# Kernel optimization log

Measured on AMD Instinct MI355X. Metric: run time of the kernel, lower is better.

## Reference

```python
import jax, jax.numpy as jnp
import numpy as np


def _species_mlp(x, W1, b1, W2, b2, W3, b3, W4, b4):
    # x: [S, A, F] per-species feature blocks; weights: [S, ...] per-species MLPs
    h = jax.nn.silu(jnp.einsum('saf,sfh->sah', x, W1) + b1[:, None, :])
    h = jax.nn.silu(jnp.einsum('sah,shk->sak', h, W2) + b2[:, None, :])
    h = jax.nn.silu(jnp.einsum('sak,skm->sam', h, W3) + b3[:, None, :])
    e = jnp.einsum('sam,smo->sao', h, W4) + b4[:, None, :]  # [S, A, 1]
    return e[..., 0]  # atomic energies [S, A]


def setup_inputs() -> dict:
    key = jax.random.key(0)
    ks = jax.random.split(key, 12)
    S, A, F, H = 4, 32768, 512, 256
    n_structures = 512
    w = 0.05  # keep activations in a sane range
    return {
        'features': jax.random.normal(ks[0], (S, A, F), dtype=jnp.float32),
        'struct_ids': jax.random.randint(ks[1], (S, A), 0, n_structures),
        'W1': jax.random.normal(ks[2], (S, F, H), dtype=jnp.float32) * w,
        'b1': jax.random.normal(ks[3], (S, H), dtype=jnp.float32) * w,
        'W2': jax.random.normal(ks[4], (S, H, H), dtype=jnp.float32) * w,
        'b2': jax.random.normal(ks[5], (S, H), dtype=jnp.float32) * w,
        'W3': jax.random.normal(ks[6], (S, H, H), dtype=jnp.float32) * w,
        'b3': jax.random.normal(ks[7], (S, H), dtype=jnp.float32) * w,
        'W4': jax.random.normal(ks[8], (S, H, 1), dtype=jnp.float32) * w,
        'b4': jax.random.normal(ks[9], (S, 1), dtype=jnp.float32) * w,
        'energy_shift': jax.random.normal(ks[10], (1,), dtype=jnp.float32),
        'n_structures': n_structures,
    }


def reference(features, struct_ids, W1, b1, W2, b2, W3, b3, W4, b4, energy_shift, n_structures):
    # per-species MLP over all blocks (the per-species gather is the block layout itself)
    atomic_energies = _species_mlp(features, W1, b1, W2, b2, W3, b3, W4, b4)  # [S, A]
    # index_add scatter of atomic energies into per-structure energies
    energies = jax.ops.segment_sum(
        atomic_energies.reshape(-1), struct_ids.reshape(-1), num_segments=n_structures
    )
    energies = energies + energy_shift[0]
    return energies
```

## Files before the change

kernel.cpp:

```cpp
#include <hip/hip_runtime.h>

typedef _Float16 f16x8 __attribute__((ext_vector_type(8)));
typedef _Float16 f16x4 __attribute__((ext_vector_type(4)));
typedef float f32x4 __attribute__((ext_vector_type(4)));

static constexpr int S = 4;
static constexpr int NATOMS = 32768;
static constexpr int FIN = 512;
static constexpr int H = 256;
static constexpr int BM = 128;
static constexpr int XSTR = 36;
static constexpr int HSTR = 264;
static constexpr int NSTRUCT = 512;
static constexpr int RBLK = 128;
static constexpr int APB = (S * NATOMS) / RBLK;

__global__ void pack_w(const float* __restrict__ W, _Float16* __restrict__ dst, int KT) {
    int idx = blockIdx.x * 256 + threadIdx.x;
    int j = idx & 7;
    int lane = (idx >> 3) & 63;
    int rest = idx >> 9;
    int kt = rest % KT;
    int t2 = rest / KT;
    int K = KT * 32;
    int k = kt * 32 + (lane >> 4) * 8 + j;
    int ntile = t2 & 15;
    int s = t2 >> 4;
    int n = ntile * 16 + (lane & 15);
    int p = kt * 4 + (ntile & 3);
    size_t o = ((((size_t)(s * 4 + (ntile >> 2))) * (KT * 4) + p) * 64 + lane) * 8 + j;
    dst[o] = (_Float16)W[((size_t)s * K + k) * H + n];
}

__global__ __launch_bounds__(512, 3) void fused_mlp(
    const float* __restrict__ X,
    const _Float16* __restrict__ W1p, const _Float16* __restrict__ W2p,
    const _Float16* __restrict__ W3p,
    const float* __restrict__ b1, const float* __restrict__ b2,
    const float* __restrict__ b3,
    const float* __restrict__ W4, const float* __restrict__ b4,
    float* __restrict__ Eout)
{
    __shared__ _Float16 smem[BM * HSTR];
    __shared__ float e_lds[4][BM];

    const int s = blockIdx.y;
    const int tile = blockIdx.x;
    const int tid = threadIdx.x;
    const int rw = __builtin_amdgcn_readfirstlane(tid >> 6);
    const int wm = rw >> 2;
    const int wn = rw & 3;
    const int lane = tid & 63;
    const int g = lane >> 4;
    const int mh = lane & 15;
    const int srow = tid >> 2;
    const int cq = tid & 3;

    const float* Xb = X + (size_t)(s * NATOMS + tile * BM) * FIN;
    _Float16* hb = smem;

    const _Float16* Wb1 = W1p + ((size_t)(s * 4 + wn)) * (64 * 512) + lane * 8;
    const _Float16* Wb2 = W2p + ((size_t)(s * 4 + wn)) * (32 * 512) + lane * 8;
    const _Float16* Wb3 = W3p + ((size_t)(s * 4 + wn)) * (32 * 512) + lane * 8;

    f32x4 acc[4][4];
#pragma unroll
    for (int i = 0; i < 4; ++i)
#pragma unroll
        for (int j = 0; j < 4; ++j)
            acc[i][j] = f32x4{0.f, 0.f, 0.f, 0.f};

    f32x4 ld[3][2];
    auto loadc = [&](int slot, int c) {
        const float* p = Xb + (size_t)srow * FIN + c * 32 + cq * 8;
        ld[slot][0] = *(const f32x4*)(p);
        ld[slot][1] = *(const f32x4*)(p + 4);
    };
    auto storec = [&](int slot, int c) {
        _Float16* xb = smem + (c % 3) * (BM * XSTR);
#pragma unroll
        for (int i = 0; i < 2; ++i) {
            f16x4 v;
#pragma unroll
            for (int j = 0; j < 4; ++j) v[j] = (_Float16)ld[slot][i][j];
            *(f16x4*)(xb + srow * XSTR + cq * 8 + i * 4) = v;
        }
    };
    auto l1mfma = [&](int c) {
        const _Float16* xb = smem + (c % 3) * (BM * XSTR);
        f16x8 a[4];
#pragma unroll
        for (int mt = 0; mt < 4; ++mt)
            a[mt] = *(const f16x8*)(xb + (wm * 64 + mt * 16 + mh) * XSTR + g * 8);
        __builtin_amdgcn_s_setprio(1);
#pragma unroll
        for (int nt = 0; nt < 4; ++nt) {
            f16x8 b = *(const f16x8*)(Wb1 + (c * 4 + nt) * 512);
#pragma unroll
            for (int mt = 0; mt < 4; ++mt)
                acc[mt][nt] = __builtin_amdgcn_mfma_f32_16x16x32_f16(a[mt], b, acc[mt][nt], 0, 0, 0);
        }
        __builtin_amdgcn_s_setprio(0);
    };

    loadc(0, 0);
    loadc(1, 1);
    loadc(2, 2);
    storec(0, 0);
    asm volatile("s_waitcnt lgkmcnt(0)" ::: "memory");
    __builtin_amdgcn_s_barrier();
#pragma unroll
    for (int c = 0; c < 16; ++c) {
        if (c < 15) storec((c + 1) % 3, c + 1);
        if (c < 13) loadc(c % 3, c + 3);
        l1mfma(c);
        asm volatile("s_waitcnt lgkmcnt(0)" ::: "memory");
        __builtin_amdgcn_s_barrier();
    }
    __syncthreads();

    {
        float bv[4];
#pragma unroll
        for (int nt = 0; nt < 4; ++nt) bv[nt] = b1[s * H + wn * 64 + nt * 16 + mh];
#pragma unroll
        for (int mt = 0; mt < 4; ++mt)
#pragma unroll
            for (int nt = 0; nt < 4; ++nt)
#pragma unroll
                for (int r = 0; r < 4; ++r) {
                    float v = acc[mt][nt][r] + bv[nt];
                    v = __fdividef(v, 1.f + __expf(-v));
                    hb[(wm * 64 + mt * 16 + g * 4 + r) * HSTR + wn * 64 + nt * 16 + mh] = (_Float16)v;
                    acc[mt][nt][r] = 0.f;
                }
    }
    __syncthreads();

    for (int l = 0; l < 2; ++l) {
        const _Float16* Wb = l ? Wb3 : Wb2;
#pragma unroll
        for (int ks = 0; ks < 8; ++ks) {
            f16x8 a[4];
#pragma unroll
            for (int mt = 0; mt < 4; ++mt)
                a[mt] = *(const f16x8*)(hb + (wm * 64 + mt * 16 + mh) * HSTR + ks * 32 + g * 8);
            __builtin_amdgcn_s_setprio(1);
#pragma unroll
            for (int nt = 0; nt < 4; ++nt) {
                f16x8 b = *(const f16x8*)(Wb + (ks * 4 + nt) * 512);
#pragma unroll
                for (int mt = 0; mt < 4; ++mt)
                    acc[mt][nt] = __builtin_amdgcn_mfma_f32_16x16x32_f16(a[mt], b, acc[mt][nt], 0, 0, 0);
            }
            __builtin_amdgcn_s_setprio(0);
        }
        __syncthreads();
        if (l == 0) {
            float bv[4];
#pragma unroll
            for (int nt = 0; nt < 4; ++nt) bv[nt] = b2[s * H + wn * 64 + nt * 16 + mh];
#pragma unroll
            for (int mt = 0; mt < 4; ++mt)
#pragma unroll
                for (int nt = 0; nt < 4; ++nt)
#pragma unroll
                    for (int r = 0; r < 4; ++r) {
                        float v = acc[mt][nt][r] + bv[nt];
                        v = __fdividef(v, 1.f + __expf(-v));
                        hb[(wm * 64 + mt * 16 + g * 4 + r) * HSTR + wn * 64 + nt * 16 + mh] = (_Float16)v;
                        acc[mt][nt][r] = 0.f;
                    }
            __syncthreads();
        }
    }

    {
        float bv[4], w4v[4];
#pragma unroll
        for (int nt = 0; nt < 4; ++nt) {
            int col = wn * 64 + nt * 16 + mh;
            bv[nt] = b3[s * H + col];
            w4v[nt] = W4[s * H + col];
        }
#pragma unroll
        for (int mt = 0; mt < 4; ++mt)
#pragma unroll
            for (int r = 0; r < 4; ++r) {
                float v = 0.f;
#pragma unroll
                for (int nt = 0; nt < 4; ++nt) {
                    float h = acc[mt][nt][r] + bv[nt];
                    h = __fdividef(h, 1.f + __expf(-h));
                    v += h * w4v[nt];
                }
                v += __shfl_xor(v, 1);
                v += __shfl_xor(v, 2);
                v += __shfl_xor(v, 4);
                v += __shfl_xor(v, 8);
                if (mh == r) e_lds[wn][wm * 64 + mt * 16 + g * 4 + r] = v;
            }
    }
    __syncthreads();
    if (tid < BM) {
        float e = b4[s] + e_lds[0][tid] + e_lds[1][tid] + e_lds[2][tid] + e_lds[3][tid];
        Eout[(size_t)s * NATOMS + tile * BM + tid] = e;
    }
}

__global__ __launch_bounds__(256) void reduce1(
    const float* __restrict__ E, const int* __restrict__ ids,
    float* __restrict__ partials)
{
    __shared__ float tbl[NSTRUCT];
    const int b = blockIdx.x;
    const int tid = threadIdx.x;
    tbl[tid] = 0.f;
    tbl[tid + 256] = 0.f;
    __syncthreads();
    const int base = b * APB;
#pragma unroll
    for (int i = 0; i < APB / 256; ++i) {
        int a = base + i * 256 + tid;
        atomicAdd(&tbl[ids[a]], E[a]);
    }
    __syncthreads();
    partials[(size_t)b * NSTRUCT + tid] = tbl[tid];
    partials[(size_t)b * NSTRUCT + tid + 256] = tbl[tid + 256];
}

__global__ __launch_bounds__(512) void reduce2(
    const float* __restrict__ partials, const float* __restrict__ shift,
    float* __restrict__ out)
{
    const int i = threadIdx.x;
    float v = shift[0];
#pragma unroll 8
    for (int b = 0; b < RBLK; ++b) v += partials[(size_t)b * NSTRUCT + i];
    out[i] = v;
}

extern "C" void kernel_launch(void* const* d_in, const int* in_sizes, int n_in,
                              void* d_out, int out_size, void* d_ws, size_t ws_size,
                              hipStream_t stream) {
    const float* X   = (const float*)d_in[0];
    const int*   ids = (const int*)d_in[1];
    const float* W1  = (const float*)d_in[2];
    const float* b1  = (const float*)d_in[3];
    const float* W2  = (const float*)d_in[4];
    const float* b2  = (const float*)d_in[5];
    const float* W3  = (const float*)d_in[6];
    const float* b3  = (const float*)d_in[7];
    const float* W4  = (const float*)d_in[8];
    const float* b4  = (const float*)d_in[9];
    const float* shift = (const float*)d_in[10];

    _Float16* W1p = (_Float16*)d_ws;
    _Float16* W2p = W1p + (size_t)S * 4 * 64 * 512;
    _Float16* W3p = W2p + (size_t)S * 4 * 32 * 512;
    float* E = (float*)(W3p + (size_t)S * 4 * 32 * 512);
    float* partials = E + (size_t)S * NATOMS;

    pack_w<<<2048, 256, 0, stream>>>(W1, W1p, 16);
    pack_w<<<1024, 256, 0, stream>>>(W2, W2p, 8);
    pack_w<<<1024, 256, 0, stream>>>(W3, W3p, 8);

    dim3 grid(NATOMS / BM, S);
    fused_mlp<<<grid, 512, 0, stream>>>(X, W1p, W2p, W3p, b1, b2, b3, W4, b4, E);

    reduce1<<<RBLK, 256, 0, stream>>>(E, ids, partials);
    reduce2<<<1, 512, 0, stream>>>(partials, shift, (float*)d_out);
}
```

Measured before the change: 155.9 us.

## Split fused MLP into separate layer-1 GEMM and layers 2-4 kernels

Splits the single fused per-tile MLP kernel into two launches. The first streams X and computes layer 1 with SiLU, writing fp16 activations to a global workspace. The second reloads those activations into LDS and runs layers 2 through 4. Each kernel now needs less LDS than the fused one, which may allow more concurrent blocks or better scheduling. The cost is an extra global write and read of a 128K x 256 fp16 activation buffer plus one more kernel launch.

```diff
diff --git a/kernel.cpp b/kernel.cpp
--- a/kernel.cpp
+++ b/kernel.cpp
@@ -32,17 +32,11 @@
     dst[o] = (_Float16)W[((size_t)s * K + k) * H + n];
 }
 
-__global__ __launch_bounds__(512, 3) void fused_mlp(
-    const float* __restrict__ X,
-    const _Float16* __restrict__ W1p, const _Float16* __restrict__ W2p,
-    const _Float16* __restrict__ W3p,
-    const float* __restrict__ b1, const float* __restrict__ b2,
-    const float* __restrict__ b3,
-    const float* __restrict__ W4, const float* __restrict__ b4,
-    float* __restrict__ Eout)
+__global__ __launch_bounds__(512, 3) void l1gemm(
+    const float* __restrict__ X, const _Float16* __restrict__ W1p,
+    const float* __restrict__ b1, _Float16* __restrict__ h1)
 {
-    __shared__ _Float16 smem[BM * HSTR];
-    __shared__ float e_lds[4][BM];
+    __shared__ _Float16 xlds[3 * BM * XSTR];
 
     const int s = blockIdx.y;
     const int tile = blockIdx.x;
@@ -57,11 +51,7 @@
     const int cq = tid & 3;
 
     const float* Xb = X + (size_t)(s * NATOMS + tile * BM) * FIN;
-    _Float16* hb = smem;
-
     const _Float16* Wb1 = W1p + ((size_t)(s * 4 + wn)) * (64 * 512) + lane * 8;
-    const _Float16* Wb2 = W2p + ((size_t)(s * 4 + wn)) * (32 * 512) + lane * 8;
-    const _Float16* Wb3 = W3p + ((size_t)(s * 4 + wn)) * (32 * 512) + lane * 8;
 
     f32x4 acc[4][4];
 #pragma unroll
@@ -77,7 +67,7 @@
         ld[slot][1] = *(const f32x4*)(p + 4);
     };
     auto storec = [&](int slot, int c) {
-        _Float16* xb = smem + (c % 3) * (BM * XSTR);
+        _Float16* xb = xlds + (c % 3) * (BM * XSTR);
 #pragma unroll
         for (int i = 0; i < 2; ++i) {
             f16x4 v;
@@ -87,7 +77,7 @@
         }
     };
     auto l1mfma = [&](int c) {
-        const _Float16* xb = smem + (c % 3) * (BM * XSTR);
+        const _Float16* xb = xlds + (c % 3) * (BM * XSTR);
         f16x8 a[4];
 #pragma unroll
         for (int mt = 0; mt < 4; ++mt)
@@ -117,25 +107,62 @@
         asm volatile("s_waitcnt lgkmcnt(0)" ::: "memory");
         __builtin_amdgcn_s_barrier();
     }
+
+    _Float16* Ho = h1 + ((size_t)(s * NATOMS + tile * BM)) * H;
+    float bv[4];
+#pragma unroll
+    for (int nt = 0; nt < 4; ++nt) bv[nt] = b1[s * H + wn * 64 + nt * 16 + mh];
+#pragma unroll
+    for (int mt = 0; mt < 4; ++mt)
+#pragma unroll
+        for (int nt = 0; nt < 4; ++nt)
+#pragma unroll
+            for (int r = 0; r < 4; ++r) {
+                float v = acc[mt][nt][r] + bv[nt];
+                v = __fdividef(v, 1.f + __expf(-v));
+                Ho[(size_t)(wm * 64 + mt * 16 + g * 4 + r) * H + wn * 64 + nt * 16 + mh] = (_Float16)v;
+            }
+}
+
+__global__ __launch_bounds__(512, 3) void l234(
+    const _Float16* __restrict__ h1,
+    const _Float16* __restrict__ W2p, const _Float16* __restrict__ W3p,
+    const float* __restrict__ b2, const float* __restrict__ b3,
+    const float* __restrict__ W4, const float* __restrict__ b4,
+    float* __restrict__ Eout)
+{
+    __shared__ _Float16 hb[BM * HSTR];
+    __shared__ float e_lds[4][BM];
+
+    const int s = blockIdx.y;
+    const int tile = blockIdx.x;
+    const int tid = threadIdx.x;
+    const int rw = __builtin_amdgcn_readfirstlane(tid >> 6);
+    const int wm = rw >> 2;
+    const int wn = rw & 3;
+    const int lane = tid & 63;
+    const int g = lane >> 4;
+    const int mh = lane & 15;
+
+    const _Float16* Wb2 = W2p + ((size_t)(s * 4 + wn)) * (32 * 512) + lane * 8;
+    const _Float16* Wb3 = W3p + ((size_t)(s * 4 + wn)) * (32 * 512) + lane * 8;
+
+    const _Float16* Hb = h1 + ((size_t)(s * NATOMS + tile * BM)) * H;
+#pragma unroll
+    for (int i = 0; i < 8; ++i) {
+        int gi = i * 512 + tid;
+        int row = gi >> 5, gr = gi & 31;
+        f16x8 v = *(const f16x8*)(Hb + (size_t)row * H + gr * 8);
+        *(f16x8*)(hb + row * HSTR + gr * 8) = v;
+    }
     __syncthreads();
 
-    {
-        float bv[4];
-#pragma unroll
-        for (int nt = 0; nt < 4; ++nt) bv[nt] = b1[s * H + wn * 64 + nt * 16 + mh];
-#pragma unroll
-        for (int mt = 0; mt < 4; ++mt)
-#pragma unroll
-            for (int nt = 0; nt < 4; ++nt)
-#pragma unroll
-                for (int r = 0; r < 4; ++r) {
-                    float v = acc[mt][nt][r] + bv[nt];
-                    v = __fdividef(v, 1.f + __expf(-v));
-                    hb[(wm * 64 + mt * 16 + g * 4 + r) * HSTR + wn * 64 + nt * 16 + mh] = (_Float16)v;
-                    acc[mt][nt][r] = 0.f;
-                }
-    }
-    __syncthreads();
+    f32x4 acc[4][4];
+#pragma unroll
+    for (int i = 0; i < 4; ++i)
+#pragma unroll
+        for (int j = 0; j < 4; ++j)
+            acc[i][j] = f32x4{0.f, 0.f, 0.f, 0.f};
 
     for (int l = 0; l < 2; ++l) {
         const _Float16* Wb = l ? Wb3 : Wb2;
@@ -260,13 +287,15 @@
     _Float16* W3p = W2p + (size_t)S * 4 * 32 * 512;
     float* E = (float*)(W3p + (size_t)S * 4 * 32 * 512);
     float* partials = E + (size_t)S * NATOMS;
+    _Float16* h1 = (_Float16*)(partials + (size_t)RBLK * NSTRUCT);
 
     pack_w<<<2048, 256, 0, stream>>>(W1, W1p, 16);
     pack_w<<<1024, 256, 0, stream>>>(W2, W2p, 8);
     pack_w<<<1024, 256, 0, stream>>>(W3, W3p, 8);
 
     dim3 grid(NATOMS / BM, S);
-    fused_mlp<<<grid, 512, 0, stream>>>(X, W1p, W2p, W3p, b1, b2, b3, W4, b4, E);
+    l1gemm<<<grid, 512, 0, stream>>>(X, W1p, b1, h1);
+    l234<<<grid, 512, 0, stream>>>(h1, W2p, W3p, b2, b3, W4, b4, E);
 
     reduce1<<<RBLK, 256, 0, stream>>>(E, ids, partials);
     reduce2<<<1, 512, 0, stream>>>(partials, shift, (float*)d_out);
```

Measured after the change: 177.6 us. +13.9%, slower.

## Switch MLP matmuls to 32x32x16 MFMA with swizzled hidden-layer LDS layout

Applied to the files above, without the earlier changes.

Replaces the 16x16x32 f16 MFMA tiling with 32x32x16 MFMA tiles (2x2 per wave), repacking weights to match the new operand layout. The hidden activation buffer in shared memory is now XOR-swizzled by row group to avoid bank conflicts on the new access pattern. The goal is fewer A/B operand loads per FLOP and higher MFMA throughput. The trade-off is larger per-lane accumulator vectors, which may raise register pressure under the 3-block launch bound, and a longer final reduction over 32 lanes.

```diff
diff --git a/kernel.cpp b/kernel.cpp
--- a/kernel.cpp
+++ b/kernel.cpp
@@ -3,6 +3,7 @@
 typedef _Float16 f16x8 __attribute__((ext_vector_type(8)));
 typedef _Float16 f16x4 __attribute__((ext_vector_type(4)));
 typedef float f32x4 __attribute__((ext_vector_type(4)));
+typedef float f32x16 __attribute__((ext_vector_type(16)));
 
 static constexpr int S = 4;
 static constexpr int NATOMS = 32768;
@@ -15,21 +16,19 @@
 static constexpr int RBLK = 128;
 static constexpr int APB = (S * NATOMS) / RBLK;
 
-__global__ void pack_w(const float* __restrict__ W, _Float16* __restrict__ dst, int KT) {
+__global__ void pack_w32(const float* __restrict__ W, _Float16* __restrict__ dst, int P) {
     int idx = blockIdx.x * 256 + threadIdx.x;
     int j = idx & 7;
     int lane = (idx >> 3) & 63;
-    int rest = idx >> 9;
-    int kt = rest % KT;
-    int t2 = rest / KT;
-    int K = KT * 32;
-    int k = kt * 32 + (lane >> 4) * 8 + j;
-    int ntile = t2 & 15;
-    int s = t2 >> 4;
-    int n = ntile * 16 + (lane & 15);
-    int p = kt * 4 + (ntile & 3);
-    size_t o = ((((size_t)(s * 4 + (ntile >> 2))) * (KT * 4) + p) * 64 + lane) * 8 + j;
-    dst[o] = (_Float16)W[((size_t)s * K + k) * H + n];
+    int p = (idx >> 9) % P;
+    int t = (idx >> 9) / P;
+    int wn = t & 3;
+    int s = t >> 2;
+    int K = P * 8;
+    int c = p >> 2, kk = (p >> 1) & 1, nt = p & 1;
+    int k = (c * 2 + kk) * 16 + (lane >> 5) * 8 + j;
+    int n = wn * 64 + nt * 32 + (lane & 31);
+    dst[((size_t)idx & ~511) + lane * 8 + j] = (_Float16)W[((size_t)s * K + k) * H + n];
 }
 
 __global__ __launch_bounds__(512, 3) void fused_mlp(
@@ -51,8 +50,8 @@
     const int wm = rw >> 2;
     const int wn = rw & 3;
     const int lane = tid & 63;
-    const int g = lane >> 4;
-    const int mh = lane & 15;
+    const int c32 = lane & 31;
+    const int hi = lane >> 5;
     const int srow = tid >> 2;
     const int cq = tid & 3;
 
@@ -63,12 +62,12 @@
     const _Float16* Wb2 = W2p + ((size_t)(s * 4 + wn)) * (32 * 512) + lane * 8;
     const _Float16* Wb3 = W3p + ((size_t)(s * 4 + wn)) * (32 * 512) + lane * 8;
 
-    f32x4 acc[4][4];
-#pragma unroll
-    for (int i = 0; i < 4; ++i)
-#pragma unroll
-        for (int j = 0; j < 4; ++j)
-            acc[i][j] = f32x4{0.f, 0.f, 0.f, 0.f};
+    f32x16 acc[2][2];
+#pragma unroll
+    for (int i = 0; i < 2; ++i)
+#pragma unroll
+        for (int j = 0; j < 2; ++j)
+            acc[i][j] = (f32x16)(0.f);
 
     f32x4 ld[3][2];
     auto loadc = [&](int slot, int c) {
@@ -88,19 +87,22 @@
     };
     auto l1mfma = [&](int c) {
         const _Float16* xb = smem + (c % 3) * (BM * XSTR);
-        f16x8 a[4];
-#pragma unroll
-        for (int mt = 0; mt < 4; ++mt)
-            a[mt] = *(const f16x8*)(xb + (wm * 64 + mt * 16 + mh) * XSTR + g * 8);
-        __builtin_amdgcn_s_setprio(1);
-#pragma unroll
-        for (int nt = 0; nt < 4; ++nt) {
-            f16x8 b = *(const f16x8*)(Wb1 + (c * 4 + nt) * 512);
-#pragma unroll
-            for (int mt = 0; mt < 4; ++mt)
-                acc[mt][nt] = __builtin_amdgcn_mfma_f32_16x16x32_f16(a[mt], b, acc[mt][nt], 0, 0, 0);
-        }
-        __builtin_amdgcn_s_setprio(0);
+#pragma unroll
+        for (int kk = 0; kk < 2; ++kk) {
+            f16x8 a[2];
+#pragma unroll
+            for (int mt = 0; mt < 2; ++mt)
+                a[mt] = *(const f16x8*)(xb + (wm * 64 + mt * 32 + c32) * XSTR + kk * 16 + hi * 8);
+            __builtin_amdgcn_s_setprio(1);
+#pragma unroll
+            for (int nt = 0; nt < 2; ++nt) {
+                f16x8 b = *(const f16x8*)(Wb1 + ((c * 4 + kk * 2 + nt)) * 512);
+#pragma unroll
+                for (int mt = 0; mt < 2; ++mt)
+                    acc[mt][nt] = __builtin_amdgcn_mfma_f32_32x32x16_f16(a[mt], b, acc[mt][nt], 0, 0, 0);
+            }
+            __builtin_amdgcn_s_setprio(0);
+        }
     };
 
     loadc(0, 0);
@@ -119,86 +121,83 @@
     }
     __syncthreads();
 
-    {
-        float bv[4];
-#pragma unroll
-        for (int nt = 0; nt < 4; ++nt) bv[nt] = b1[s * H + wn * 64 + nt * 16 + mh];
-#pragma unroll
-        for (int mt = 0; mt < 4; ++mt)
-#pragma unroll
-            for (int nt = 0; nt < 4; ++nt)
-#pragma unroll
-                for (int r = 0; r < 4; ++r) {
-                    float v = acc[mt][nt][r] + bv[nt];
+    auto hwrite = [&](int grow, int col, float v) {
+        int g8 = (col >> 3) ^ ((grow >> 3) & 3);
+        hb[grow * HSTR + (g8 << 3) + (col & 7)] = (_Float16)v;
+    };
+    auto silu_epi = [&](const float* bias) {
+#pragma unroll
+        for (int nt = 0; nt < 2; ++nt) {
+            float bv = bias[s * H + wn * 64 + nt * 32 + c32];
+#pragma unroll
+            for (int mt = 0; mt < 2; ++mt)
+#pragma unroll
+                for (int r = 0; r < 16; ++r) {
+                    float v = acc[mt][nt][r] + bv;
                     v = __fdividef(v, 1.f + __expf(-v));
-                    hb[(wm * 64 + mt * 16 + g * 4 + r) * HSTR + wn * 64 + nt * 16 + mh] = (_Float16)v;
+                    int grow = wm * 64 + mt * 32 + (r & 3) + 8 * (r >> 2) + 4 * hi;
+                    hwrite(grow, wn * 64 + nt * 32 + c32, v);
                     acc[mt][nt][r] = 0.f;
                 }
-    }
+        }
+    };
+
+    silu_epi(b1);
     __syncthreads();
 
     for (int l = 0; l < 2; ++l) {
         const _Float16* Wb = l ? Wb3 : Wb2;
 #pragma unroll
         for (int ks = 0; ks < 8; ++ks) {
-            f16x8 a[4];
-#pragma unroll
-            for (int mt = 0; mt < 4; ++mt)
-                a[mt] = *(const f16x8*)(hb + (wm * 64 + mt * 16 + mh) * HSTR + ks * 32 + g * 8);
-            __builtin_amdgcn_s_setprio(1);
-#pragma unroll
-            for (int nt = 0; nt < 4; ++nt) {
-                f16x8 b = *(const f16x8*)(Wb + (ks * 4 + nt) * 512);
-#pragma unroll
-                for (int mt = 0; mt < 4; ++mt)
-                    acc[mt][nt] = __builtin_amdgcn_mfma_f32_16x16x32_f16(a[mt], b, acc[mt][nt], 0, 0, 0);
+#pragma unroll
+            for (int kk = 0; kk < 2; ++kk) {
+                f16x8 a[2];
+#pragma unroll
+                for (int mt = 0; mt < 2; ++mt) {
+                    int grow = wm * 64 + mt * 32 + c32;
+                    int g8 = (ks * 4 + kk * 2 + hi) ^ ((grow >> 3) & 3);
+                    a[mt] = *(const f16x8*)(hb + grow * HSTR + (g8 << 3));
+                }
+                __builtin_amdgcn_s_setprio(1);
+#pragma unroll
+                for (int nt = 0; nt < 2; ++nt) {
+                    f16x8 b = *(const f16x8*)(Wb + ((ks * 4 + kk * 2 + nt)) * 512);
+#pragma unroll
+                    for (int mt = 0; mt < 2; ++mt)
+                        acc[mt][nt] = __builtin_amdgcn_mfma_f32_32x32x16_f16(a[mt], b, acc[mt][nt], 0, 0, 0);
+                }
+                __builtin_amdgcn_s_setprio(0);
             }
-            __builtin_amdgcn_s_setprio(0);
         }
         __syncthreads();
         if (l == 0) {
-            float bv[4];
-#pragma unroll
-            for (int nt = 0; nt < 4; ++nt) bv[nt] = b2[s * H + wn * 64 + nt * 16 + mh];
-#pragma unroll
-            for (int mt = 0; mt < 4; ++mt)
-#pragma unroll
-                for (int nt = 0; nt < 4; ++nt)
-#pragma unroll
-                    for (int r = 0; r < 4; ++r) {
-                        float v = acc[mt][nt][r] + bv[nt];
-                        v = __fdividef(v, 1.f + __expf(-v));
-                        hb[(wm * 64 + mt * 16 + g * 4 + r) * HSTR + wn * 64 + nt * 16 + mh] = (_Float16)v;
-                        acc[mt][nt][r] = 0.f;
-                    }
+            silu_epi(b2);
             __syncthreads();
         }
     }
 
     {
-        float bv[4], w4v[4];
-#pragma unroll
-        for (int nt = 0; nt < 4; ++nt) {
-            int col = wn * 64 + nt * 16 + mh;
-            bv[nt] = b3[s * H + col];
-            w4v[nt] = W4[s * H + col];
-        }
-#pragma unroll
-        for (int mt = 0; mt < 4; ++mt)
-#pragma unroll
-            for (int r = 0; r < 4; ++r) {
+#pragma unroll
+        for (int mt = 0; mt < 2; ++mt)
+#pragma unroll
+            for (int r = 0; r < 16; ++r) {
                 float v = 0.f;
 #pragma unroll
-                for (int nt = 0; nt < 4; ++nt) {
-                    float h = acc[mt][nt][r] + bv[nt];
+                for (int nt = 0; nt < 2; ++nt) {
+                    int col = wn * 64 + nt * 32 + c32;
+                    float h = acc[mt][nt][r] + b3[s * H + col];
                     h = __fdividef(h, 1.f + __expf(-h));
-                    v += h * w4v[nt];
+                    v += h * W4[s * H + col];
                 }
                 v += __shfl_xor(v, 1);
                 v += __shfl_xor(v, 2);
                 v += __shfl_xor(v, 4);
                 v += __shfl_xor(v, 8);
-                if (mh == r) e_lds[wn][wm * 64 + mt * 16 + g * 4 + r] = v;
+                v += __shfl_xor(v, 16);
+                if (c32 == r) {
+                    int grow = wm * 64 + mt * 32 + (r & 3) + 8 * (r >> 2) + 4 * hi;
+                    e_lds[wn][grow] = v;
+                }
             }
     }
     __syncthreads();
@@ -261,9 +260,9 @@
     float* E = (float*)(W3p + (size_t)S * 4 * 32 * 512);
     float* partials = E + (size_t)S * NATOMS;
 
-    pack_w<<<2048, 256, 0, stream>>>(W1, W1p, 16);
-    pack_w<<<1024, 256, 0, stream>>>(W2, W2p, 8);
-    pack_w<<<1024, 256, 0, stream>>>(W3, W3p, 8);
+    pack_w32<<<2048, 256, 0, stream>>>(W1, W1p, 64);
+    pack_w32<<<1024, 256, 0, stream>>>(W2, W2p, 32);
+    pack_w32<<<1024, 256, 0, stream>>>(W3, W3p, 32);
 
     dim3 grid(NATOMS / BM, S);
     fused_mlp<<<grid, 512, 0, stream>>>(X, W1p, W2p, W3p, b1, b2, b3, W4, b4, E);
```

Result: slower. 167.8 us (+7.7%).

## Prefetch layer-1 MFMA operands into double-buffered registers and merge weight packing

Applied to the files above, without the earlier changes.

The first-layer loop now keeps the LDS activation fragments and the packed W1 fragments for the next chunk in double-buffered registers. These loads are issued before the current chunk's MFMAs, so load latency overlaps compute. The LDS staging now runs two chunks ahead instead of one. The three weight-packing launches are merged into a single kernel, and the fused kernel's launch-bounds occupancy hint drops from 3 to 2 blocks, which gives more registers per thread but less latency hiding from occupancy.

```diff
diff --git a/kernel.cpp b/kernel.cpp
--- a/kernel.cpp
+++ b/kernel.cpp
@@ -15,8 +15,18 @@
 static constexpr int RBLK = 128;
 static constexpr int APB = (S * NATOMS) / RBLK;
 
-__global__ void pack_w(const float* __restrict__ W, _Float16* __restrict__ dst, int KT) {
-    int idx = blockIdx.x * 256 + threadIdx.x;
+__global__ void pack_all(const float* __restrict__ W1, const float* __restrict__ W2,
+                         const float* __restrict__ W3,
+                         _Float16* __restrict__ W1p, _Float16* __restrict__ W2p,
+                         _Float16* __restrict__ W3p) {
+    int bid = blockIdx.x;
+    const float* W;
+    _Float16* dst;
+    int KT, base;
+    if (bid < 2048)      { W = W1; dst = W1p; KT = 16; base = 0; }
+    else if (bid < 3072) { W = W2; dst = W2p; KT = 8;  base = 2048; }
+    else                 { W = W3; dst = W3p; KT = 8;  base = 3072; }
+    int idx = (bid - base) * 256 + threadIdx.x;
     int j = idx & 7;
     int lane = (idx >> 3) & 63;
     int rest = idx >> 9;
@@ -32,7 +42,7 @@
     dst[o] = (_Float16)W[((size_t)s * K + k) * H + n];
 }
 
-__global__ __launch_bounds__(512, 3) void fused_mlp(
+__global__ __launch_bounds__(512, 2) void fused_mlp(
     const float* __restrict__ X,
     const _Float16* __restrict__ W1p, const _Float16* __restrict__ W2p,
     const _Float16* __restrict__ W3p,
@@ -86,20 +96,27 @@
             *(f16x4*)(xb + srow * XSTR + cq * 8 + i * 4) = v;
         }
     };
+
+    f16x8 areg[2][4];
+    f16x8 wr[2][4];
+    auto aread = [&](int c) {
+        const _Float16* xb = smem + (c % 3) * (BM * XSTR);
+#pragma unroll
+        for (int mt = 0; mt < 4; ++mt)
+            areg[c & 1][mt] = *(const f16x8*)(xb + (wm * 64 + mt * 16 + mh) * XSTR + g * 8);
+    };
+    auto wread = [&](int c) {
+#pragma unroll
+        for (int nt = 0; nt < 4; ++nt)
+            wr[c & 1][nt] = *(const f16x8*)(Wb1 + (c * 4 + nt) * 512);
+    };
     auto l1mfma = [&](int c) {
-        const _Float16* xb = smem + (c % 3) * (BM * XSTR);
-        f16x8 a[4];
-#pragma unroll
-        for (int mt = 0; mt < 4; ++mt)
-            a[mt] = *(const f16x8*)(xb + (wm * 64 + mt * 16 + mh) * XSTR + g * 8);
         __builtin_amdgcn_s_setprio(1);
 #pragma unroll
-        for (int nt = 0; nt < 4; ++nt) {
-            f16x8 b = *(const f16x8*)(Wb1 + (c * 4 + nt) * 512);
+        for (int nt = 0; nt < 4; ++nt)
 #pragma unroll
             for (int mt = 0; mt < 4; ++mt)
-                acc[mt][nt] = __builtin_amdgcn_mfma_f32_16x16x32_f16(a[mt], b, acc[mt][nt], 0, 0, 0);
-        }
+                acc[mt][nt] = __builtin_amdgcn_mfma_f32_16x16x32_f16(areg[c & 1][mt], wr[c & 1][nt], acc[mt][nt], 0, 0, 0);
         __builtin_amdgcn_s_setprio(0);
     };
 
@@ -107,12 +124,19 @@
     loadc(1, 1);
     loadc(2, 2);
     storec(0, 0);
+    storec(1, 1);
+    wread(0);
     asm volatile("s_waitcnt lgkmcnt(0)" ::: "memory");
     __builtin_amdgcn_s_barrier();
+    aread(0);
 #pragma unroll
     for (int c = 0; c < 16; ++c) {
-        if (c < 15) storec((c + 1) % 3, c + 1);
-        if (c < 13) loadc(c % 3, c + 3);
+        if (c < 14) storec((c + 2) % 3, c + 2);
+        if (c < 13) loadc((c + 3) % 3, c + 3);
+        if (c < 15) {
+            wread(c + 1);
+            aread(c + 1);
+        }
         l1mfma(c);
         asm volatile("s_waitcnt lgkmcnt(0)" ::: "memory");
         __builtin_amdgcn_s_barrier();
@@ -261,9 +285,7 @@
     float* E = (float*)(W3p + (size_t)S * 4 * 32 * 512);
     float* partials = E + (size_t)S * NATOMS;
 
-    pack_w<<<2048, 256, 0, stream>>>(W1, W1p, 16);
-    pack_w<<<1024, 256, 0, stream>>>(W2, W2p, 8);
-    pack_w<<<1024, 256, 0, stream>>>(W3, W3p, 8);
+    pack_all<<<4096, 256, 0, stream>>>(W1, W2, W3, W1p, W2p, W3p);
 
     dim3 grid(NATOMS / BM, S);
     fused_mlp<<<grid, 512, 0, stream>>>(X, W1p, W2p, W3p, b1, b2, b3, W4, b4, E);
```

Measured after the change: 183.5 us. 17.7% more time.
